# Kernel optimization log

Measured on AMD Instinct MI355X. Metric: run time of the kernel, lower is better.

The kernel has to match this reference:

```python
import jax, jax.numpy as jnp
import numpy as np

B, N, E, Dh, L = 64, 128, 1024, 300, 2  # batch, num_utter, emb_dim, hidden_dim, gnn_layers


def gru_cell(x, h, wih, whh, bih, bhh):
    # torch.nn.GRUCell math; gate order r, z, n
    gi = x @ wih.T + bih
    gh = h @ whh.T + bhh
    ir, iz, inn = jnp.split(gi, 3, axis=-1)
    hr, hz, hn = jnp.split(gh, 3, axis=-1)
    r = jax.nn.sigmoid(ir + hr)
    z = jax.nn.sigmoid(iz + hz)
    n = jnp.tanh(inn + r * hn)
    return (1.0 - z) * n + z * h


def dag_layer(Hl, mask, wg, bg, cwih, cwhh, cbih, cbhh, pwih, pwhh, pbih, pbhh):
    # Hl: (B,N,Dh); mask: (B,N,N) strict-causal DAG adjacency (float 0/1)
    wq, wk = wg[:Dh], wg[Dh:]  # GatLinear: Linear(2*Dh, 1) split over [Q; K]
    x0 = Hl[:, 0]
    z0 = jnp.zeros_like(x0)
    C0 = gru_cell(x0, z0, cwih, cwhh, cbih, cbhh)  # grus_c(H0, hx=None)
    P0 = gru_cell(z0, x0, pwih, pwhh, pbih, pbhh)  # grus_p(M=0, H0)
    buf0 = jnp.zeros_like(Hl).at[:, 0].set(C0 + P0)

    xs = (jnp.swapaxes(Hl[:, 1:], 0, 1),      # (N-1,B,Dh)
          jnp.swapaxes(mask[:, 1:], 0, 1),    # (N-1,B,N)
          jnp.arange(1, Hl.shape[1]))

    def step(buf, inp):
        x, m, i = inp  # x:(B,Dh), m:(B,N) allows only positions j<i with adj==1
        alpha = (x @ wq)[:, None] + buf @ wk + bg        # (B,N) additive score
        alpha = alpha - (1.0 - m) * 1e30                 # mask_logic
        w = jax.nn.softmax(alpha, axis=-1)
        M = jnp.einsum('bn,bnd->bd', w, buf)             # attn_sum over history H1
        C = gru_cell(x, M, cwih, cwhh, cbih, cbhh)       # grus_c(H_i, M)
        P = gru_cell(M, x, pwih, pwhh, pbih, pbhh)       # grus_p(M, H_i)
        return buf.at[:, i].set(C + P), None

    buf, _ = jax.lax.scan(step, buf0, xs)
    return buf


def setup_inputs():
    key = jax.random.key(0)
    ks = jax.random.split(key, 16)
    features = jax.random.normal(ks[0], (B, N, E), jnp.float32)
    adj = jax.random.randint(ks[1], (B, N, N), 0, 2, dtype=jnp.int32)
    idx = jnp.arange(1, N)
    adj = adj.at[:, idx, idx - 1].set(1)  # every utterance links to its predecessor (valid DAG)
    s_mask = jax.random.randint(ks[2], (B, N, N), 0, 2, dtype=jnp.int32)
    s_mask_onehot = jax.nn.one_hot(s_mask, 2, dtype=jnp.int32)
    lengths = jnp.full((B,), N, dtype=jnp.int32)
    s = 0.05
    return {
        'features': features,
        'fc1_w': jax.random.normal(ks[3], (E, Dh), jnp.float32) * s,
        'fc1_b': jnp.zeros((Dh,), jnp.float32),
        'gat_w': jax.random.normal(ks[4], (L, 2 * Dh), jnp.float32) * s,
        'gat_b': jnp.zeros((L,), jnp.float32),
        'gc_wih': jax.random.normal(ks[5], (L, 3 * Dh, Dh), jnp.float32) * s,
        'gc_whh': jax.random.normal(ks[6], (L, 3 * Dh, Dh), jnp.float32) * s,
        'gc_bih': jnp.zeros((L, 3 * Dh), jnp.float32),
        'gc_bhh': jnp.zeros((L, 3 * Dh), jnp.float32),
        'gp_wih': jax.random.normal(ks[7], (L, 3 * Dh, Dh), jnp.float32) * s,
        'gp_whh': jax.random.normal(ks[8], (L, 3 * Dh, Dh), jnp.float32) * s,
        'gp_bih': jnp.zeros((L, 3 * Dh), jnp.float32),
        'gp_bhh': jnp.zeros((L, 3 * Dh), jnp.float32),
        'adj': adj,
        's_mask': s_mask,
        's_mask_onehot': s_mask_onehot,
        'lengths': lengths,
    }


def reference(features, fc1_w, fc1_b, gat_w, gat_b, gc_wih, gc_whh, gc_bih, gc_bhh,
              gp_wih, gp_whh, gp_bih, gp_bhh, adj, s_mask, s_mask_onehot, lengths):
    H0 = jax.nn.relu(features @ fc1_w + fc1_b)                 # (B,N,Dh)
    causal = jnp.tril(jnp.ones((N, N), features.dtype), k=-1)  # strictly past (j<i)
    mask = adj.astype(features.dtype) * causal                 # adj[:, i, :i]
    Hs = [H0]
    Hl = H0
    for l in range(L):
        Hl = dag_layer(Hl, mask, gat_w[l], gat_b[l],
                       gc_wih[l], gc_whh[l], gc_bih[l], gc_bhh[l],
                       gp_wih[l], gp_whh[l], gp_bih[l], gp_bhh[l])
        Hs.append(Hl)
    Hs.append(features)
    # nodal_att_type=None -> attentive_node_features is identity; module returns H
    return jnp.concatenate(Hs, axis=2)  # (B,N,Dh*(L+1)+E)
```

## Files before the change

kernel.cpp:

```cpp
#include <hip/hip_runtime.h>
#include <hip/hip_fp16.h>

#define B_   64
#define NB   128
#define E_   1024
#define DH   300
#define G3   900
#define G6   1800
#define OUTD 1924
#define SLICES 4
#define PK_STRIDE 1800
#define MROW 160
#define BROWS 1856

typedef _Float16 h2raw __attribute__((ext_vector_type(2)));
typedef _Float16 f16x8 __attribute__((ext_vector_type(8)));
typedef float f32x4 __attribute__((ext_vector_type(4)));

__device__ __forceinline__ float dot2f(unsigned int m2, unsigned int w, float acc) {
    h2raw a, b;
    __builtin_memcpy(&a, &m2, 4);
    __builtin_memcpy(&b, &w, 4);
    return __builtin_amdgcn_fdot2(a, b, acc, false);
}

__device__ __forceinline__ unsigned int packh2(float x, float y) {
    __half2 h;
    h.x = __float2half_rn(x);
    h.y = __float2half_rn(y);
    unsigned int u;
    __builtin_memcpy(&u, &h, 4);
    return u;
}

__device__ __forceinline__ float sigmoidf_(float x) { return 1.f / (1.f + __expf(-x)); }
__device__ __forceinline__ float tanh_fast(float x) { return 1.f - 2.f / (__expf(2.f * x) + 1.f); }

__global__ __launch_bounds__(256)
void copy_feat(const float* __restrict__ f, float* __restrict__ out) {
    const long id = (long)blockIdx.x * 256 + threadIdx.x;
    const long r = id >> 8;
    const int  c = (int)(id & 255);
    const float4 v = ((const float4*)(f + r * E_))[c];
    ((float4*)(out + r * OUTD + 3 * DH))[c] = v;
}

__global__ __launch_bounds__(256)
void pack2(const float* __restrict__ gc_whh, const float* __restrict__ gp_wih,
           unsigned int* __restrict__ dst) {
    const int id = blockIdx.x * 256 + threadIdx.x;
    if (id >= 2 * 150 * PK_STRIDE) return;
    const int l   = id / (150 * PK_STRIDE);
    const int rem = id % (150 * PK_STRIDE);
    const int kp  = rem / PK_STRIDE;
    const int R   = rem % PK_STRIDE;
    const int mat = R / G3;
    const int o   = R % G3;
    const float* W = (mat ? gp_wih : gc_whh) + (long)l * G3 * DH;
    const float2 v = *(const float2*)(W + (long)o * DH + 2 * kp);
    dst[id] = packh2(v.x, v.y);
}

__global__ __launch_bounds__(256)
void pack_af(const float* __restrict__ src, unsigned int* __restrict__ dst) {
    const long id = (long)blockIdx.x * 256 + threadIdx.x;
    const long r = id >> 9;
    const int kp = (int)(id & 511);
    const float2 v = *(const float2*)(src + r * E_ + 2 * kp);
    dst[id] = packh2(v.x, v.y);
}

__global__ __launch_bounds__(256)
void pack_bf(const float* __restrict__ W, unsigned int* __restrict__ dst) {
    const int id = blockIdx.x * 256 + threadIdx.x;
    const int n = id >> 9;
    const int kp = id & 511;
    unsigned int u = 0u;
    if (n < DH) u = packh2(W[(2 * kp) * DH + n], W[(2 * kp + 1) * DH + n]);
    dst[id] = u;
}

__global__ __launch_bounds__(256)
void pack_bw2(const float* __restrict__ Wc, const float* __restrict__ Wp,
              unsigned int* __restrict__ dst) {
    const int id = blockIdx.x * 256 + threadIdx.x;
    if (id >= 2 * BROWS * 160) return;
    const int l   = id / (BROWS * 160);
    const int rem = id % (BROWS * 160);
    const int n   = rem / 160;
    const int kp  = rem % 160;
    unsigned int u = 0u;
    if (n < G6 && kp < 150) {
        const float* W = (n < G3 ? Wc : Wp) + (long)l * G3 * DH;
        const int o = (n < G3) ? n : n - G3;
        const float2 v = *(const float2*)(W + (long)o * DH + 2 * kp);
        u = packh2(v.x, v.y);
    }
    dst[id] = u;
}

__device__ __forceinline__ f16x8 ldfrag(const unsigned int* p) {
    const uint4 u = *(const uint4*)p;
    f16x8 r;
    __builtin_memcpy(&r, &u, 16);
    return r;
}

template<int RELU, int PACKOUT>
__global__ __launch_bounds__(256)
void gemm_mf(const unsigned int* __restrict__ APK, int ldap,
             const unsigned int* __restrict__ BPK, int ldbp,
             const float* __restrict__ bias1, const float* __restrict__ bias2, int bsplit,
             float* __restrict__ C, int ldc,
             unsigned int* __restrict__ CPK, int ldcp,
             int N, int KSTEPS)
{
    const int lane = threadIdx.x & 63;
    const int wv = threadIdx.x >> 6;
    const int m0 = blockIdx.y * 128 + wv * 32;
    const int n0 = blockIdx.x * 64;
    const int ln = lane & 15;
    const int lh = lane >> 4;

    const unsigned int* a0p = APK + (long)(m0 + ln) * ldap + lh * 4;
    const unsigned int* a1p = a0p + 16L * ldap;
    const unsigned int* b0p = BPK + (long)(n0 + ln) * ldbp + lh * 4;

    f32x4 acc[2][4];
    #pragma unroll
    for (int mi = 0; mi < 2; ++mi)
        #pragma unroll
        for (int bj = 0; bj < 4; ++bj)
            acc[mi][bj] = (f32x4){0.f, 0.f, 0.f, 0.f};

    for (int ks = 0; ks < KSTEPS; ++ks) {
        const int off = ks * 16;
        const f16x8 a0 = ldfrag(a0p + off);
        const f16x8 a1 = ldfrag(a1p + off);
        const f16x8 b0 = ldfrag(b0p + off);
        const f16x8 b1 = ldfrag(b0p + 16L * ldbp + off);
        const f16x8 b2 = ldfrag(b0p + 32L * ldbp + off);
        const f16x8 b3 = ldfrag(b0p + 48L * ldbp + off);
        acc[0][0] = __builtin_amdgcn_mfma_f32_16x16x32_f16(a0, b0, acc[0][0], 0, 0, 0);
        acc[0][1] = __builtin_amdgcn_mfma_f32_16x16x32_f16(a0, b1, acc[0][1], 0, 0, 0);
        acc[0][2] = __builtin_amdgcn_mfma_f32_16x16x32_f16(a0, b2, acc[0][2], 0, 0, 0);
        acc[0][3] = __builtin_amdgcn_mfma_f32_16x16x32_f16(a0, b3, acc[0][3], 0, 0, 0);
        acc[1][0] = __builtin_amdgcn_mfma_f32_16x16x32_f16(a1, b0, acc[1][0], 0, 0, 0);
        acc[1][1] = __builtin_amdgcn_mfma_f32_16x16x32_f16(a1, b1, acc[1][1], 0, 0, 0);
        acc[1][2] = __builtin_amdgcn_mfma_f32_16x16x32_f16(a1, b2, acc[1][2], 0, 0, 0);
        acc[1][3] = __builtin_amdgcn_mfma_f32_16x16x32_f16(a1, b3, acc[1][3], 0, 0, 0);
    }

    #pragma unroll
    for (int mi = 0; mi < 2; ++mi) {
        #pragma unroll
        for (int bj = 0; bj < 4; ++bj) {
            const int gcol = n0 + bj * 16 + ln;
            #pragma unroll
            for (int r = 0; r < 4; ++r) {
                const int gm = m0 + mi * 16 + lh * 4 + r;
                float v = acc[mi][bj][r];
                if (gcol < N) v += (gcol < bsplit) ? bias1[gcol] : bias2[gcol - bsplit];
                if (RELU) v = fmaxf(v, 0.f);
                const float pr = PACKOUT ? __shfl_xor(v, 1) : 0.f;
                if (gcol < N) {
                    C[(long)gm * ldc + gcol] = v;
                    if (PACKOUT && !(ln & 1))
                        CPK[(long)gm * ldcp + (gcol >> 1)] = packh2(v, pr);
                }
            }
        }
    }
}

__global__ __launch_bounds__(512, 2)
void scan14(float* __restrict__ out,
            const float* __restrict__ GG,
            const unsigned int* __restrict__ PK2L,
            const float* __restrict__ cbhh,
            const float* __restrict__ pbih,
            const int* __restrict__ adj,
            const float* __restrict__ wk,
            unsigned long long* __restrict__ TBL,
            unsigned int* __restrict__ APKN,
            int l)
{
    extern __shared__ unsigned int histp[];
    __shared__ float wsm2[NB];
    __shared__ float betas[NB];
    __shared__ float Mlds[DH];
    __shared__ __align__(16) unsigned int M2[152];
    __shared__ float gmv[456];
    __shared__ float mx2s, S_pres;

    const int tid = threadIdx.x;
    const int lane = tid & 63;
    const int wid = tid >> 6;
    const int b = blockIdx.x & 63;
    const int k = blockIdx.x >> 6;
    const int swk = (k == 3) ? 72 : 76;

    float* outb = out + (long)b * NB * OUTD;
    const float* xcol = outb + l * DH;
    float* ycol = outb + (l + 1) * DH;
    const float* ggb = GG + (long)b * NB * G6;
    const int* adjb = adj + b * NB * NB;
    unsigned long long* mb = TBL + (long)b * NB * MROW;
    unsigned int* mb32 = (unsigned int*)mb;

    if (tid < 152) M2[tid] = 0u;

    const int D = 76 * k + ((tid < swk) ? tid : 0);
    const float cb0 = cbhh[D], cb1 = cbhh[DH + D], cb2 = cbhh[2 * DH + D];
    const float pb0 = pbih[D], pb1 = pbih[DH + D], pb2 = pbih[2 * DH + D];
    const float wkD = wk[D];

    const int ROWS = 6 * swk;
    int R;
    {
        const int t = (tid < ROWS) ? tid : 0;
        const int d = t % swk;
        const int r = t / swk;
        R = (r / 3) * G3 + (r % 3) * DH + 76 * k + d;
    }
    unsigned int w[152];
    #pragma unroll
    for (int j = 0; j < 150; ++j) w[j] = PK2L[j * PK_STRIDE + R];
    w[150] = 0u; w[151] = 0u;

    __syncthreads();

    const bool isv = (tid >= 256) && (tid < 406);
    const int vt = tid - 256;

    for (int i = 0; i < NB; ++i) {
        float gi0 = 0, gi1 = 0, gi2 = 0, gp0 = 0, gp1 = 0, gp2 = 0, xi = 0;
        if (tid < swk) {
            const float* gic = ggb + (long)i * G6;
            gi0 = gic[D]; gi1 = gic[DH + D]; gi2 = gic[2 * DH + D];
            gp0 = gic[G3 + D]; gp1 = gic[G3 + DH + D]; gp2 = gic[G3 + 2 * DH + D];
            xi = xcol[(long)i * OUTD + D];
        }
        int a0p = 0, a1p = 0;
        if (wid == 2 && i + 1 < NB) {
            a0p = adjb[(i + 1) * NB + lane];
            a1p = adjb[(i + 1) * NB + 64 + lane];
        }

        if (i > 0) {
            float V0 = 0.f, V1 = 0.f;
            if (wid == 0) {
                const unsigned long long* trow = mb + (long)(i - 1) * MROW;
                const unsigned int tag = (unsigned int)i;
                const bool act = (lane < 8);
                unsigned long long tv = 0;
                while (true) {
                    if (act && (unsigned int)tv != tag)
                        tv = __hip_atomic_load(&trow[152 + lane],
                                               __ATOMIC_RELAXED, __HIP_MEMORY_SCOPE_AGENT);
                    if (__all(!act || (unsigned int)tv == tag)) break;
                }
                unsigned long long d0 = 0, d1 = 0;
                if (lane < 38) {
                    d0 = __hip_atomic_load(&trow[2 * lane],
                                           __ATOMIC_RELAXED, __HIP_MEMORY_SCOPE_AGENT);
                    d1 = __hip_atomic_load(&trow[2 * lane + 1],
                                           __ATOMIC_RELAXED, __HIP_MEMORY_SCOPE_AGENT);
                }
                float bp = 0.f;
                if (act) {
                    const unsigned int hb = (unsigned int)(tv >> 32);
                    __builtin_memcpy(&bp, &hb, 4);
                }
                bp += __shfl_xor(bp, 1);
                bp += __shfl_xor(bp, 2);
                bp += __shfl_xor(bp, 4);
                if (lane == 0) betas[i - 1] = __shfl(bp, 0);

                if (lane < 38) {
                    uint4 q;
                    q.x = (unsigned int)d0; q.y = (unsigned int)(d0 >> 32);
                    q.z = (unsigned int)d1; q.w = (unsigned int)(d1 >> 32);
                    *(uint4*)&histp[(i - 1) * 152 + 4 * lane] = q;
                }
            } else if (isv) {
                #pragma unroll 4
                for (int j = 0; j + 1 < i; ++j) {
                    const float wj = wsm2[j];
                    const unsigned int u = histp[j * 152 + vt];
                    __half2 h; __builtin_memcpy(&h, &u, 4);
                    V0 = fmaf(wj, __half2float(h.x), V0);
                    V1 = fmaf(wj, __half2float(h.y), V1);
                }
            }
            __syncthreads();

            if (isv) {
                const float beta_new = betas[i - 1];
                const float mxl = mx2s;
                float S = S_pres, e;
                if (beta_new > mxl) {
                    const float sc = __expf(mxl - beta_new);
                    V0 *= sc; V1 *= sc; S *= sc; e = 1.f;
                } else {
                    e = __expf(beta_new - mxl);
                }
                const unsigned int u = histp[(i - 1) * 152 + vt];
                __half2 h; __builtin_memcpy(&h, &u, 4);
                S += e;
                V0 = fmaf(e, __half2float(h.x), V0);
                V1 = fmaf(e, __half2float(h.y), V1);
                const float inv = 1.f / S;
                const float m0 = V0 * inv, m1 = V1 * inv;
                Mlds[2 * vt] = m0;
                Mlds[2 * vt + 1] = m1;
                M2[vt] = packh2(m0, m1);
            }
        } else {
            if (tid < DH) Mlds[tid] = 0.f;
        }
        __syncthreads();

        if (tid < ROWS) {
            float a0 = 0.f, a1 = 0.f;
            #pragma unroll
            for (int j4 = 0; j4 < 152; j4 += 4) {
                const uint4 m4 = *(const uint4*)&M2[j4];
                a0 = dot2f(m4.x, w[j4 + 0], a0);
                a1 = dot2f(m4.y, w[j4 + 1], a1);
                a0 = dot2f(m4.z, w[j4 + 2], a0);
                a1 = dot2f(m4.w, w[j4 + 3], a1);
            }
            gmv[tid] = a0 + a1;
        }
        __syncthreads();

        if (wid < 2) {
            float rowv = 0.f;
            if (tid < swk) {
                const float Mi = Mlds[D];
                const float hc0 = gmv[0 * swk + tid] + cb0;
                const float hc1 = gmv[1 * swk + tid] + cb1;
                const float hc2 = gmv[2 * swk + tid] + cb2;
                const float rc = sigmoidf_(gi0 + hc0);
                const float zc = sigmoidf_(gi1 + hc1);
                const float nc = tanh_fast(gi2 + rc * hc2);
                const float Cc = (1.f - zc) * nc + zc * Mi;
                const float ip0 = gmv[3 * swk + tid] + pb0;
                const float ip1 = gmv[4 * swk + tid] + pb1;
                const float ip2 = gmv[5 * swk + tid] + pb2;
                const float rp = sigmoidf_(ip0 + gp0);
                const float zp = sigmoidf_(ip1 + gp1);
                const float np = tanh_fast(ip2 + rp * gp2);
                const float Pp = (1.f - zp) * np + zp * xi;
                rowv = Cc + Pp;
            }
            const float pr = __shfl_xor(rowv, 1);
            const unsigned int pairu32 = packh2(rowv, pr);
            if (tid < swk && !(tid & 1)) {
                __hip_atomic_store(&mb32[(long)i * (MROW * 2) + 38 * k + (tid >> 1)], pairu32,
                                   __ATOMIC_RELAXED, __HIP_MEMORY_SCOPE_AGENT);
                if (l == 0)
                    APKN[((long)b * NB + i) * 160 + 38 * k + (tid >> 1)] = pairu32;
            }
            float bv = (tid < swk) ? rowv * wkD : 0.f;
            #pragma unroll
            for (int off = 32; off; off >>= 1) bv += __shfl_xor(bv, off);
            asm volatile("s_waitcnt vmcnt(0)" ::: "memory");
            if (lane == 0) {
                unsigned int bbits;
                __builtin_memcpy(&bbits, &bv, 4);
                const unsigned long long pkt =
                    ((unsigned long long)bbits << 32) | (unsigned int)(i + 1);
                __hip_atomic_store(&mb[(long)i * MROW + 152 + 2 * k + wid], pkt,
                                   __ATOMIC_RELAXED, __HIP_MEMORY_SCOPE_AGENT);
            }
            if (tid < swk) ycol[(long)i * OUTD + D] = rowv;
        } else if (wid == 2 && i + 1 < NB) {
            const int j1 = lane + 64;
            const bool v0 = (lane < i) && (a0p != 0);
            const bool v1 = (j1 < i) && (a1p != 0);
            const float aa0 = v0 ? betas[lane] : -3.0e38f;
            const float aa1 = v1 ? betas[j1]   : -3.0e38f;
            float mx = fmaxf(aa0, aa1);
            #pragma unroll
            for (int off = 32; off; off >>= 1) mx = fmaxf(mx, __shfl_xor(mx, off));
            const float e0 = v0 ? __expf(aa0 - mx) : 0.f;
            const float e1 = v1 ? __expf(aa1 - mx) : 0.f;
            float s = e0 + e1;
            #pragma unroll
            for (int off = 32; off; off >>= 1) s += __shfl_xor(s, off);
            wsm2[lane] = e0;
            wsm2[j1]   = e1;
            if (lane == 0) { mx2s = mx; S_pres = s; }
        }
        __syncthreads();
    }
}

extern "C" void kernel_launch(void* const* d_in, const int* in_sizes, int n_in,
                              void* d_out, int out_size, void* d_ws, size_t ws_size,
                              hipStream_t stream) {
    (void)in_sizes; (void)n_in; (void)out_size; (void)ws_size;
    const float* features = (const float*)d_in[0];
    const float* fc1_w    = (const float*)d_in[1];
    const float* fc1_b    = (const float*)d_in[2];
    const float* gat_w    = (const float*)d_in[3];
    const float* gc_wih   = (const float*)d_in[5];
    const float* gc_whh   = (const float*)d_in[6];
    const float* gc_bih   = (const float*)d_in[7];
    const float* gc_bhh   = (const float*)d_in[8];
    const float* gp_wih   = (const float*)d_in[9];
    const float* gp_whh   = (const float*)d_in[10];
    const float* gp_bih   = (const float*)d_in[11];
    const float* gp_bhh   = (const float*)d_in[12];
    const int*   adj      = (const int*)d_in[13];
    float* out = (float*)d_out;

    unsigned long long* TB = (unsigned long long*)d_ws;
    float* GG = (float*)(TB + 2L * B_ * NB * MROW);
    unsigned int* PK2  = (unsigned int*)(GG + 8192L * G6);
    unsigned int* APK2 = PK2 + 2 * 150 * PK_STRIDE;
    unsigned int* BPKF = APK2 + 8192L * 160;
    unsigned int* BPKL = BPKF + 320L * 512;
    unsigned int* APK1 = (unsigned int*)GG;

    hipFuncSetAttribute(reinterpret_cast<const void*>(scan14),
                        hipFuncAttributeMaxDynamicSharedMemorySize, 80000);
    hipMemsetAsync(TB, 0, 2L * B_ * NB * MROW * sizeof(unsigned long long), stream);
    hipMemsetAsync(APK2, 0, 8192L * 160 * sizeof(unsigned int), stream);

    copy_feat<<<dim3((B_ * NB * E_) / 1024), 256, 0, stream>>>(features, out);
    pack2<<<dim3((2 * 150 * PK_STRIDE + 255) / 256), 256, 0, stream>>>(gc_whh, gp_wih, PK2);

    pack_af<<<dim3(8192 * 512 / 256), 256, 0, stream>>>(features, APK1);
    pack_bf<<<dim3(320 * 512 / 256), 256, 0, stream>>>(fc1_w, BPKF);
    pack_bw2<<<dim3((2 * BROWS * 160 + 255) / 256), 256, 0, stream>>>(gc_wih, gp_whh, BPKL);

    gemm_mf<1, 1><<<dim3(5, 64), 256, 0, stream>>>(
        APK1, 512, BPKF, 512, fc1_b, fc1_b, DH, out, OUTD, APK2, 160, DH, 32);

    for (int l = 0; l < 2; ++l) {
        gemm_mf<0, 0><<<dim3(29, 64), 256, 0, stream>>>(
            APK2, 160, BPKL + (long)l * BROWS * 160, 160,
            gc_bih + l * G3, gp_bhh + l * G3, G3,
            GG, G6, (unsigned int*)nullptr, 0, G6, 10);
        scan14<<<dim3(SLICES * B_), 512, 77824, stream>>>(
            out, GG, PK2 + (long)l * 150 * PK_STRIDE,
            gc_bhh + l * G3, gp_bih + l * G3, adj,
            gat_w + l * 2 * DH + DH,
            TB + (long)l * B_ * NB * MROW,
            APK2, l);
    }
}
```

Measured before the change: 1.099 ms.

## Merge packing kernels into one launch and split scan weights into transposed vector loads

Replaces the five packing and copy kernels and the APK2 memset with a single pack_all kernel that also zeroes only the padding columns of APK2. It adds a row-major transposed fp16 copy of the first 76 packed K-pairs of the recurrent weights, so each scan thread loads half its weights with contiguous uint4 loads instead of strided scalar loads. The remaining half stays in a separate array, apparently so register pressure or spilling can be managed. This cuts launch count and memset traffic and speeds the scan prologue's weight load, at the cost of extra workspace and a larger single kernel with branchy segment dispatch.

```diff
diff --git a/kernel.cpp b/kernel.cpp
--- a/kernel.cpp
+++ b/kernel.cpp
@@ -36,67 +36,98 @@
 __device__ __forceinline__ float sigmoidf_(float x) { return 1.f / (1.f + __expf(-x)); }
 __device__ __forceinline__ float tanh_fast(float x) { return 1.f - 2.f / (__expf(2.f * x) + 1.f); }
 
+#define NA (2 * 150 * PK_STRIDE)
+#define NB_SEG (8192 * 512)
+#define NC (320 * 512)
+#define ND (2 * BROWS * 160)
+#define NE (2 * 1800 * 76)
+#define NF (B_ * NB * 256)
+#define NG (8192 * 10)
+#define NTOT (NA + NB_SEG + NC + ND + NE + NF + NG)
+
 __global__ __launch_bounds__(256)
-void copy_feat(const float* __restrict__ f, float* __restrict__ out) {
-    const long id = (long)blockIdx.x * 256 + threadIdx.x;
-    const long r = id >> 8;
-    const int  c = (int)(id & 255);
-    const float4 v = ((const float4*)(f + r * E_))[c];
-    ((float4*)(out + r * OUTD + 3 * DH))[c] = v;
-}
-
-__global__ __launch_bounds__(256)
-void pack2(const float* __restrict__ gc_whh, const float* __restrict__ gp_wih,
-           unsigned int* __restrict__ dst) {
-    const int id = blockIdx.x * 256 + threadIdx.x;
-    if (id >= 2 * 150 * PK_STRIDE) return;
-    const int l   = id / (150 * PK_STRIDE);
-    const int rem = id % (150 * PK_STRIDE);
-    const int kp  = rem / PK_STRIDE;
-    const int R   = rem % PK_STRIDE;
-    const int mat = R / G3;
-    const int o   = R % G3;
-    const float* W = (mat ? gp_wih : gc_whh) + (long)l * G3 * DH;
-    const float2 v = *(const float2*)(W + (long)o * DH + 2 * kp);
-    dst[id] = packh2(v.x, v.y);
-}
-
-__global__ __launch_bounds__(256)
-void pack_af(const float* __restrict__ src, unsigned int* __restrict__ dst) {
-    const long id = (long)blockIdx.x * 256 + threadIdx.x;
-    const long r = id >> 9;
-    const int kp = (int)(id & 511);
-    const float2 v = *(const float2*)(src + r * E_ + 2 * kp);
-    dst[id] = packh2(v.x, v.y);
-}
-
-__global__ __launch_bounds__(256)
-void pack_bf(const float* __restrict__ W, unsigned int* __restrict__ dst) {
-    const int id = blockIdx.x * 256 + threadIdx.x;
-    const int n = id >> 9;
-    const int kp = id & 511;
-    unsigned int u = 0u;
-    if (n < DH) u = packh2(W[(2 * kp) * DH + n], W[(2 * kp + 1) * DH + n]);
-    dst[id] = u;
-}
-
-__global__ __launch_bounds__(256)
-void pack_bw2(const float* __restrict__ Wc, const float* __restrict__ Wp,
-              unsigned int* __restrict__ dst) {
-    const int id = blockIdx.x * 256 + threadIdx.x;
-    if (id >= 2 * BROWS * 160) return;
-    const int l   = id / (BROWS * 160);
-    const int rem = id % (BROWS * 160);
-    const int n   = rem / 160;
-    const int kp  = rem % 160;
-    unsigned int u = 0u;
-    if (n < G6 && kp < 150) {
-        const float* W = (n < G3 ? Wc : Wp) + (long)l * G3 * DH;
-        const int o = (n < G3) ? n : n - G3;
+void pack_all(const float* __restrict__ gc_whh, const float* __restrict__ gp_wih,
+              const float* __restrict__ features, const float* __restrict__ fc1_w,
+              const float* __restrict__ gc_wih, const float* __restrict__ gp_whh,
+              unsigned int* __restrict__ PK2, unsigned int* __restrict__ APK1,
+              unsigned int* __restrict__ BPKF, unsigned int* __restrict__ BPKL,
+              unsigned int* __restrict__ PK2T, float* __restrict__ out,
+              unsigned int* __restrict__ APK2)
+{
+    long id = (long)blockIdx.x * 256 + threadIdx.x;
+    if (id >= NTOT) return;
+    if (id < NA) {
+        const int l   = (int)(id / (150 * PK_STRIDE));
+        const int rem = (int)(id % (150 * PK_STRIDE));
+        const int kp  = rem / PK_STRIDE;
+        const int R   = rem % PK_STRIDE;
+        const int mat = R / G3;
+        const int o   = R % G3;
+        const float* W = (mat ? gp_wih : gc_whh) + (long)l * G3 * DH;
         const float2 v = *(const float2*)(W + (long)o * DH + 2 * kp);
-        u = packh2(v.x, v.y);
-    }
-    dst[id] = u;
+        PK2[id] = packh2(v.x, v.y);
+        return;
+    }
+    id -= NA;
+    if (id < NB_SEG) {
+        const long r = id >> 9;
+        const int kp = (int)(id & 511);
+        const float2 v = *(const float2*)(features + r * E_ + 2 * kp);
+        APK1[id] = packh2(v.x, v.y);
+        return;
+    }
+    id -= NB_SEG;
+    if (id < NC) {
+        const int n = (int)(id >> 9);
+        const int kp = (int)(id & 511);
+        unsigned int u = 0u;
+        if (n < DH) u = packh2(fc1_w[(2 * kp) * DH + n], fc1_w[(2 * kp + 1) * DH + n]);
+        BPKF[id] = u;
+        return;
+    }
+    id -= NC;
+    if (id < ND) {
+        const int l   = (int)(id / (BROWS * 160));
+        const int rem = (int)(id % (BROWS * 160));
+        const int n   = rem / 160;
+        const int kp  = rem % 160;
+        unsigned int u = 0u;
+        if (n < G6 && kp < 150) {
+            const float* W = (n < G3 ? gc_wih : gp_whh) + (long)l * G3 * DH;
+            const int o = (n < G3) ? n : n - G3;
+            const float2 v = *(const float2*)(W + (long)o * DH + 2 * kp);
+            u = packh2(v.x, v.y);
+        }
+        BPKL[id] = u;
+        return;
+    }
+    id -= ND;
+    if (id < NE) {
+        const int l   = (int)(id / (1800 * 76));
+        const int rem = (int)(id % (1800 * 76));
+        const int R   = rem / 76;
+        const int kp  = rem % 76;
+        const int mat = R / G3;
+        const int o   = R % G3;
+        const float* W = (mat ? gp_wih : gc_whh) + (long)l * G3 * DH;
+        const float2 v = *(const float2*)(W + (long)o * DH + 2 * kp);
+        PK2T[id] = packh2(v.x, v.y);
+        return;
+    }
+    id -= NE;
+    if (id < NF) {
+        const long r = id >> 8;
+        const int  c = (int)(id & 255);
+        const float4 v = ((const float4*)(features + r * E_))[c];
+        ((float4*)(out + r * OUTD + 3 * DH))[c] = v;
+        return;
+    }
+    id -= NF;
+    {
+        const long r = id / 10;
+        const int c = (int)(id % 10);
+        APK2[r * 160 + 150 + c] = 0u;
+    }
 }
 
 __device__ __forceinline__ f16x8 ldfrag(const unsigned int* p) {
@@ -174,9 +205,10 @@
 }
 
 __global__ __launch_bounds__(512, 2)
-void scan14(float* __restrict__ out,
+void scan16(float* __restrict__ out,
             const float* __restrict__ GG,
             const unsigned int* __restrict__ PK2L,
+            const unsigned int* __restrict__ PK2TL,
             const float* __restrict__ cbhh,
             const float* __restrict__ pbih,
             const int* __restrict__ adj,
@@ -223,10 +255,16 @@
         const int r = t / swk;
         R = (r / 3) * G3 + (r % 3) * DH + 76 * k + d;
     }
-    unsigned int w[152];
+    uint4 wr[19];
+    {
+        const unsigned int* pkt = PK2TL + (long)R * 76;
+        #pragma unroll
+        for (int q = 0; q < 19; ++q) wr[q] = *(const uint4*)(pkt + 4 * q);
+    }
+    unsigned int ws[76];
     #pragma unroll
-    for (int j = 0; j < 150; ++j) w[j] = PK2L[j * PK_STRIDE + R];
-    w[150] = 0u; w[151] = 0u;
+    for (int j = 0; j < 76; ++j)
+        ws[j] = (j < 74) ? PK2L[(76 + j) * PK_STRIDE + R] : 0u;
 
     __syncthreads();
 
@@ -324,12 +362,21 @@
         if (tid < ROWS) {
             float a0 = 0.f, a1 = 0.f;
             #pragma unroll
-            for (int j4 = 0; j4 < 152; j4 += 4) {
-                const uint4 m4 = *(const uint4*)&M2[j4];
-                a0 = dot2f(m4.x, w[j4 + 0], a0);
-                a1 = dot2f(m4.y, w[j4 + 1], a1);
-                a0 = dot2f(m4.z, w[j4 + 2], a0);
-                a1 = dot2f(m4.w, w[j4 + 3], a1);
+            for (int q = 0; q < 19; ++q) {
+                const uint4 m4 = *(const uint4*)&M2[4 * q];
+                a0 = dot2f(m4.x, wr[q].x, a0);
+                a1 = dot2f(m4.y, wr[q].y, a1);
+                a0 = dot2f(m4.z, wr[q].z, a0);
+                a1 = dot2f(m4.w, wr[q].w, a1);
+            }
+            #pragma unroll
+            for (int q = 0; q < 19; ++q) {
+                const uint4 m4 = *(const uint4*)&M2[76 + 4 * q];
+                const uint4 w4 = *(const uint4*)&ws[4 * q];
+                a0 = dot2f(m4.x, w4.x, a0);
+                a1 = dot2f(m4.y, w4.y, a1);
+                a0 = dot2f(m4.z, w4.z, a0);
+                a1 = dot2f(m4.w, w4.w, a1);
             }
             gmv[tid] = a0 + a1;
         }
@@ -423,19 +470,16 @@
     unsigned int* APK2 = PK2 + 2 * 150 * PK_STRIDE;
     unsigned int* BPKF = APK2 + 8192L * 160;
     unsigned int* BPKL = BPKF + 320L * 512;
+    unsigned int* PK2T = BPKL + 2L * BROWS * 160;
     unsigned int* APK1 = (unsigned int*)GG;
 
-    hipFuncSetAttribute(reinterpret_cast<const void*>(scan14),
+    hipFuncSetAttribute(reinterpret_cast<const void*>(scan16),
                         hipFuncAttributeMaxDynamicSharedMemorySize, 80000);
     hipMemsetAsync(TB, 0, 2L * B_ * NB * MROW * sizeof(unsigned long long), stream);
-    hipMemsetAsync(APK2, 0, 8192L * 160 * sizeof(unsigned int), stream);
-
-    copy_feat<<<dim3((B_ * NB * E_) / 1024), 256, 0, stream>>>(features, out);
-    pack2<<<dim3((2 * 150 * PK_STRIDE + 255) / 256), 256, 0, stream>>>(gc_whh, gp_wih, PK2);
-
-    pack_af<<<dim3(8192 * 512 / 256), 256, 0, stream>>>(features, APK1);
-    pack_bf<<<dim3(320 * 512 / 256), 256, 0, stream>>>(fc1_w, BPKF);
-    pack_bw2<<<dim3((2 * BROWS * 160 + 255) / 256), 256, 0, stream>>>(gc_wih, gp_whh, BPKL);
+
+    pack_all<<<dim3((NTOT + 255) / 256), 256, 0, stream>>>(
+        gc_whh, gp_wih, features, fc1_w, gc_wih, gp_whh,
+        PK2, APK1, BPKF, BPKL, PK2T, out, APK2);
 
     gemm_mf<1, 1><<<dim3(5, 64), 256, 0, stream>>>(
         APK1, 512, BPKF, 512, fc1_b, fc1_b, DH, out, OUTD, APK2, 160, DH, 32);
@@ -445,8 +489,9 @@
             APK2, 160, BPKL + (long)l * BROWS * 160, 160,
             gc_bih + l * G3, gp_bhh + l * G3, G3,
             GG, G6, (unsigned int*)nullptr, 0, G6, 10);
-        scan14<<<dim3(SLICES * B_), 512, 77824, stream>>>(
+        scan16<<<dim3(SLICES * B_), 512, 77824, stream>>>(
             out, GG, PK2 + (long)l * 150 * PK_STRIDE,
+            PK2T + (long)l * 1800 * 76,
             gc_bhh + l * G3, gp_bih + l * G3, adj,
             gat_w + l * 2 * DH + DH,
             TB + (long)l * B_ * NB * MROW,
```

New measurement: 1.076 ms. 2.1% less time.
